# Kernel tuning notes

Measured on AMD Instinct MI355X. Metric: run time of the kernel, lower is better.

## Reference

```python
import jax, jax.numpy as jnp
import numpy as np

B, N, D, H = 4, 2048, 512, 8
HD = D // H


def setup_inputs() -> dict:
    key = jax.random.key(0)
    ks = jax.random.split(key, 12)
    s = 1.0 / np.sqrt(D)
    return {
        "node_feat": jax.random.normal(ks[0], (B, N, D), jnp.float32),
        "edge_weights": jax.random.uniform(ks[1], (B, N, N), jnp.float32),
        "adj_matrix": jax.random.uniform(ks[2], (B, N, N), jnp.float32),
        "masks": jnp.ones((B, N), jnp.float32),
        "class_token": 0.02 * jax.random.normal(ks[3], (1, 1, D), jnp.float32),
        "Wq": jax.random.uniform(ks[4], (D, D), jnp.float32, -s, s),
        "bq": jnp.zeros((D,), jnp.float32),
        "Wk": jax.random.uniform(ks[5], (D, D), jnp.float32, -s, s),
        "bk": jnp.zeros((D,), jnp.float32),
        "Wv": jax.random.uniform(ks[6], (D, D), jnp.float32, -s, s),
        "bv": jnp.zeros((D,), jnp.float32),
        "Wo": jax.random.uniform(ks[7], (D, D), jnp.float32, -s, s),
        "bo": jnp.zeros((D,), jnp.float32),
        "gamma": jnp.ones((D,), jnp.float32),
        "beta": jnp.zeros((D,), jnp.float32),
    }


def _attn_mask(edge_weights, masks):
    # inner block: edge gates + self-loops, clamped at 1
    inner = jnp.minimum(edge_weights + jnp.eye(N, dtype=edge_weights.dtype), 1.0)
    top = jnp.concatenate([jnp.ones((B, 1, 1), edge_weights.dtype), masks[:, None, :]], axis=2)  # [B,1,1+N]
    bot = jnp.concatenate([jnp.ones((B, N, 1), edge_weights.dtype), inner], axis=2)              # [B,N,1+N]
    m = jnp.concatenate([top, bot], axis=1)  # [B,1+N,1+N]
    ext = jnp.concatenate([jnp.ones((B, 1), masks.dtype), masks], axis=1)  # [B,1+N], CLS always valid
    return m * ext[:, None, :] * ext[:, :, None]


def reference(node_feat, edge_weights, adj_matrix, masks, class_token,
              Wq, bq, Wk, bk, Wv, bv, Wo, bo, gamma, beta):
    x = jnp.concatenate([jnp.broadcast_to(class_token, (B, 1, D)), node_feat], axis=1)  # [B,1+N,D]
    S = 1 + N
    q = (x @ Wq.T + bq).reshape(B, S, H, HD).transpose(0, 2, 1, 3)
    k = (x @ Wk.T + bk).reshape(B, S, H, HD).transpose(0, 2, 1, 3)
    v = (x @ Wv.T + bv).reshape(B, S, H, HD).transpose(0, 2, 1, 3)
    scores = jnp.einsum('bhqd,bhkd->bhqk', q, k) / jnp.sqrt(jnp.float32(HD))
    m = _attn_mask(edge_weights, masks)
    scores = jnp.where(m[:, None, :, :] == 0, jnp.float32(-1e9), scores)
    attn = jax.nn.softmax(scores, axis=-1)
    out = jnp.einsum('bhqk,bhkd->bhqd', attn, v).transpose(0, 2, 1, 3).reshape(B, S, D)
    out = out @ Wo.T + bo
    y = out + x
    mu = jnp.mean(y, axis=-1, keepdims=True)
    var = jnp.mean((y - mu) ** 2, axis=-1, keepdims=True)
    y = (y - mu) / jnp.sqrt(var + 1e-5) * gamma + beta
    return y[:, 0, :]
```

## Files before the change

### kernel.cpp

```cpp
#include <hip/hip_runtime.h>

#define B_ 4
#define N_ 2048
#define D_ 512
#define H_ 8
#define S_ (N_ + 1)
#define SC 32
#define NCH 65

#define Q0_OFF   0
#define TQ_OFF   1024
#define ATTN_OFF 8192
#define PW_OFF   81920
#define PZ_OFF   (PW_OFF + NCH * B_ * H_ * D_)
#define W_OFF    (PZ_OFF + NCH * B_ * H_ + 32)
#define O0_OFF   (W_OFF + B_ * H_ * D_)
#define Y_OFF    (O0_OFF + B_ * D_)

__device__ __forceinline__ float wave_reduce_sum(float v) {
    #pragma unroll
    for (int off = 32; off > 0; off >>= 1) v += __shfl_down(v, off, 64);
    return v;
}
__device__ __forceinline__ float wave_allreduce_sum(float v) {
    #pragma unroll
    for (int off = 1; off < 64; off <<= 1) v += __shfl_xor(v, off, 64);
    return v;
}

__global__ void q0_kernel(const float* __restrict__ ct,
                          const float* __restrict__ Wq, const float* __restrict__ bq,
                          float* __restrict__ ws) {
    int wv = threadIdx.x >> 6, lane = threadIdx.x & 63;
    int r = blockIdx.x * 8 + wv;
    const float4* c4 = (const float4*)ct;
    float4 ca = c4[lane * 2], cb = c4[lane * 2 + 1];
    const float4* row = (const float4*)(Wq + (size_t)r * D_);
    float4 a = row[lane * 2], b = row[lane * 2 + 1];
    float acc = a.x*ca.x + a.y*ca.y + a.z*ca.z + a.w*ca.w
              + b.x*cb.x + b.y*cb.y + b.z*cb.z + b.w*cb.w;
    acc = wave_reduce_sum(acc);
    if (lane == 0) ws[Q0_OFF + r] = acc + bq[r];
}

__global__ void tq_kernel(const float* __restrict__ Wk, float* __restrict__ ws) {
    int h = blockIdx.x, jc = blockIdx.y;
    int tid = threadIdx.x;
    __shared__ float q0s[64];
    if (tid < 64) q0s[tid] = ws[Q0_OFF + h * 64 + tid];
    __syncthreads();
    int j = jc * 128 + tid;
    float acc = 0.f;
    #pragma unroll 8
    for (int d2 = 0; d2 < 64; ++d2)
        acc += q0s[d2] * Wk[(size_t)(h * 64 + d2) * D_ + j];
    ws[TQ_OFF + h * D_ + j] = acc;
}

__global__ void __launch_bounds__(512)
scores_kernel(const float* __restrict__ nf, const float* __restrict__ ct,
              const float* __restrict__ masks, float* __restrict__ ws) {
    int b = blockIdx.y;
    int wv = threadIdx.x >> 6, lane = threadIdx.x & 63;
    int s = blockIdx.x * 8 + wv;
    if (s >= S_) return;
    const float* xrow = (s == 0) ? ct : (nf + ((size_t)b * N_ + (s - 1)) * D_);
    const float4* x4 = (const float4*)xrow;
    float4 xa = x4[lane];
    float4 xb = x4[64 + lane];
    float gate = 1.0f;
    if (s > 0) gate = (masks[b * N_ + s - 1] != 0.0f) ? 1.0f : 0.0f;
    const float4* t4 = (const float4*)(ws + TQ_OFF);
    float p[H_];
    #pragma unroll
    for (int h = 0; h < H_; ++h) {
        float4 ta = t4[h * 128 + lane], tb = t4[h * 128 + 64 + lane];
        p[h] = ta.x*xa.x + ta.y*xa.y + ta.z*xa.z + ta.w*xa.w
             + tb.x*xb.x + tb.y*xb.y + tb.z*xb.z + tb.w*xb.w;
        p[h] = wave_allreduce_sum(p[h]);
    }
    if (lane == 0) {
        #pragma unroll
        for (int h = 0; h < H_; ++h)
            ws[ATTN_OFF + (size_t)(b * H_ + h) * S_ + s] = gate * __expf(p[h] * 0.125f);
    }
}

__global__ void __launch_bounds__(512)
wsum_kernel(const float* __restrict__ nf, const float* __restrict__ ct,
            float* __restrict__ ws) {
    int chunk = blockIdx.x, b = blockIdx.y;
    int tid = threadIdx.x;
    __shared__ float sa[H_][SC];
    int s0 = chunk * SC;
    if (tid < H_ * SC) {
        int h = tid >> 5, ss = tid & 31;
        int s = s0 + ss;
        sa[h][ss] = (s < S_) ? ws[ATTN_OFF + (size_t)(b * H_ + h) * S_ + s] : 0.f;
    }
    __syncthreads();
    float acc[H_];
    #pragma unroll
    for (int h = 0; h < H_; ++h) acc[h] = 0.f;
    int smax = min(SC, S_ - s0);
    for (int ss = 0; ss < smax; ++ss) {
        int s = s0 + ss;
        const float* xrow = (s == 0) ? ct : (nf + ((size_t)b * N_ + (s - 1)) * D_);
        float xv = xrow[tid];
        #pragma unroll
        for (int h = 0; h < H_; ++h) acc[h] += sa[h][ss] * xv;
    }
    size_t base = ((size_t)chunk * B_ + b) * H_;
    #pragma unroll
    for (int h = 0; h < H_; ++h)
        ws[PW_OFF + (base + h) * D_ + tid] = acc[h];
    if (tid < H_) {
        float z = 0.f;
        #pragma unroll 8
        for (int ss = 0; ss < SC; ++ss) z += sa[tid][ss];
        ws[PZ_OFF + base + tid] = z;
    }
}

__global__ void reduce_w_kernel(float* __restrict__ ws) {
    int bh = blockIdx.x;
    int j = blockIdx.y * 128 + threadIdx.x;
    float z = 0.f;
    #pragma unroll 5
    for (int c = 0; c < NCH; ++c) z += ws[PZ_OFF + (size_t)(c * B_ * H_) + bh];
    float acc = 0.f;
    #pragma unroll 5
    for (int c = 0; c < NCH; ++c)
        acc += ws[PW_OFF + ((size_t)(c * B_ * H_) + bh) * D_ + j];
    ws[W_OFF + (size_t)bh * D_ + j] = acc / z;
}

__global__ void wv_kernel(const float* __restrict__ Wv, const float* __restrict__ bv,
                          float* __restrict__ ws) {
    int b = blockIdx.x;
    int wv = threadIdx.x >> 6, lane = threadIdx.x & 63;
    int r = blockIdx.y * 4 + wv;
    const float4* wrow = (const float4*)(ws + W_OFF + (size_t)b * H_ * D_ + (size_t)(r >> 6) * D_);
    float4 wa = wrow[lane * 2], wb = wrow[lane * 2 + 1];
    const float4* row = (const float4*)(Wv + (size_t)r * D_);
    float4 a = row[lane * 2], c = row[lane * 2 + 1];
    float acc = a.x*wa.x + a.y*wa.y + a.z*wa.z + a.w*wa.w
              + c.x*wb.x + c.y*wb.y + c.z*wb.z + c.w*wb.w;
    acc = wave_reduce_sum(acc);
    if (lane == 0) ws[O0_OFF + b * D_ + r] = acc + bv[r];
}

__global__ void wo_kernel(const float* __restrict__ Wo, const float* __restrict__ bo,
                          const float* __restrict__ ct, float* __restrict__ ws) {
    int b = blockIdx.x;
    int wv = threadIdx.x >> 6, lane = threadIdx.x & 63;
    int r = blockIdx.y * 4 + wv;
    const float4* ov = (const float4*)(ws + O0_OFF + (size_t)b * D_);
    float4 oa = ov[lane * 2], ob = ov[lane * 2 + 1];
    const float4* row = (const float4*)(Wo + (size_t)r * D_);
    float4 a = row[lane * 2], c = row[lane * 2 + 1];
    float acc = a.x*oa.x + a.y*oa.y + a.z*oa.z + a.w*oa.w
              + c.x*ob.x + c.y*ob.y + c.z*ob.z + c.w*ob.w;
    acc = wave_reduce_sum(acc);
    if (lane == 0) ws[Y_OFF + b * D_ + r] = acc + bo[r] + ct[r];
}

__global__ void ln_kernel(const float* __restrict__ gamma, const float* __restrict__ beta,
                          const float* __restrict__ ws, float* __restrict__ out) {
    int b = blockIdx.x;
    int tid = threadIdx.x, wv = tid >> 6, lane = tid & 63;
    float v = ws[Y_OFF + b * D_ + tid];
    float s1 = v, s2 = v * v;
    #pragma unroll
    for (int off = 32; off > 0; off >>= 1) {
        s1 += __shfl_down(s1, off, 64);
        s2 += __shfl_down(s2, off, 64);
    }
    __shared__ float r1[8], r2[8];
    if (lane == 0) { r1[wv] = s1; r2[wv] = s2; }
    __syncthreads();
    if (tid == 0) {
        float a = 0.f, c = 0.f;
        for (int i = 0; i < 8; ++i) { a += r1[i]; c += r2[i]; }
        r1[0] = a; r2[0] = c;
    }
    __syncthreads();
    float mean = r1[0] * (1.0f / D_);
    float var  = r2[0] * (1.0f / D_) - mean * mean;
    float rinv = rsqrtf(var + 1e-5f);
    out[b * D_ + tid] = (v - mean) * rinv * gamma[tid] + beta[tid];
}

extern "C" void kernel_launch(void* const* d_in, const int* in_sizes, int n_in,
                              void* d_out, int out_size, void* d_ws, size_t ws_size,
                              hipStream_t stream) {
    const float* nf    = (const float*)d_in[0];
    const float* masks = (const float*)d_in[3];
    const float* ct    = (const float*)d_in[4];
    const float* Wq    = (const float*)d_in[5];
    const float* bq    = (const float*)d_in[6];
    const float* Wk    = (const float*)d_in[7];
    const float* Wv    = (const float*)d_in[9];
    const float* bv    = (const float*)d_in[10];
    const float* Wo    = (const float*)d_in[11];
    const float* bo    = (const float*)d_in[12];
    const float* gamma = (const float*)d_in[13];
    const float* beta  = (const float*)d_in[14];
    float* ws  = (float*)d_ws;
    float* out = (float*)d_out;

    hipLaunchKernelGGL(q0_kernel, dim3(64), dim3(512), 0, stream, ct, Wq, bq, ws);
    hipLaunchKernelGGL(tq_kernel, dim3(H_, 4), dim3(128), 0, stream, Wk, ws);
    hipLaunchKernelGGL(scores_kernel, dim3(257, B_), dim3(512), 0, stream, nf, ct, masks, ws);
    hipLaunchKernelGGL(wsum_kernel, dim3(NCH, B_), dim3(512), 0, stream, nf, ct, ws);
    hipLaunchKernelGGL(reduce_w_kernel, dim3(B_ * H_, 4), dim3(128), 0, stream, ws);
    hipLaunchKernelGGL(wv_kernel, dim3(B_, 128), dim3(256), 0, stream, Wv, bv, ws);
    hipLaunchKernelGGL(wo_kernel, dim3(B_, 128), dim3(256), 0, stream, Wo, bo, ct, ws);
    hipLaunchKernelGGL(ln_kernel, dim3(B_), dim3(512), 0, stream, gamma, beta, ws, out);
}
```

Measured before the change: 189.0 us.

## Fuse all stages into one persistent kernel with software grid barriers

```diff
diff --git a/kernel.cpp b/kernel.cpp
--- a/kernel.cpp
+++ b/kernel.cpp
@@ -7,14 +7,15 @@
 #define S_ (N_ + 1)
 #define SC 32
 #define NCH 65
-
-#define Q0_OFF   0
+#define NB  260
+
+#define BAR_OFF  0
+#define Q0_OFF   64
 #define TQ_OFF   1024
 #define ATTN_OFF 8192
 #define PW_OFF   81920
 #define PZ_OFF   (PW_OFF + NCH * B_ * H_ * D_)
-#define W_OFF    (PZ_OFF + NCH * B_ * H_ + 32)
-#define O0_OFF   (W_OFF + B_ * H_ * D_)
+#define O0_OFF   (PZ_OFF + 2176)
 #define Y_OFF    (O0_OFF + B_ * D_)
 
 __device__ __forceinline__ float wave_reduce_sum(float v) {
@@ -27,168 +28,194 @@
     for (int off = 1; off < 64; off <<= 1) v += __shfl_xor(v, off, 64);
     return v;
 }
-
-__global__ void q0_kernel(const float* __restrict__ ct,
-                          const float* __restrict__ Wq, const float* __restrict__ bq,
-                          float* __restrict__ ws) {
-    int wv = threadIdx.x >> 6, lane = threadIdx.x & 63;
-    int r = blockIdx.x * 8 + wv;
-    const float4* c4 = (const float4*)ct;
-    float4 ca = c4[lane * 2], cb = c4[lane * 2 + 1];
-    const float4* row = (const float4*)(Wq + (size_t)r * D_);
-    float4 a = row[lane * 2], b = row[lane * 2 + 1];
-    float acc = a.x*ca.x + a.y*ca.y + a.z*ca.z + a.w*ca.w
-              + b.x*cb.x + b.y*cb.y + b.z*cb.z + b.w*cb.w;
-    acc = wave_reduce_sum(acc);
-    if (lane == 0) ws[Q0_OFF + r] = acc + bq[r];
-}
-
-__global__ void tq_kernel(const float* __restrict__ Wk, float* __restrict__ ws) {
-    int h = blockIdx.x, jc = blockIdx.y;
-    int tid = threadIdx.x;
-    __shared__ float q0s[64];
-    if (tid < 64) q0s[tid] = ws[Q0_OFF + h * 64 + tid];
-    __syncthreads();
-    int j = jc * 128 + tid;
-    float acc = 0.f;
-    #pragma unroll 8
-    for (int d2 = 0; d2 < 64; ++d2)
-        acc += q0s[d2] * Wk[(size_t)(h * 64 + d2) * D_ + j];
-    ws[TQ_OFF + h * D_ + j] = acc;
+__device__ __forceinline__ float dot8(float4 a, float4 b, float4 c, float4 d) {
+    return a.x*b.x + a.y*b.y + a.z*b.z + a.w*b.w
+         + c.x*d.x + c.y*d.y + c.z*d.z + c.w*d.w;
+}
+
+__device__ __forceinline__ void grid_barrier(unsigned* bar, unsigned tgt) {
+    __syncthreads();
+    if (threadIdx.x == 0) {
+        __threadfence();
+        __hip_atomic_fetch_add(bar, 1u, __ATOMIC_RELEASE, __HIP_MEMORY_SCOPE_AGENT);
+        while (__hip_atomic_load(bar, __ATOMIC_ACQUIRE, __HIP_MEMORY_SCOPE_AGENT) < tgt) {
+            __builtin_amdgcn_s_sleep(1);
+        }
+    }
+    __syncthreads();
+}
+
+__global__ void init_kernel(float* __restrict__ ws) {
+    if (threadIdx.x < 32) ((unsigned*)ws)[BAR_OFF + threadIdx.x] = 0u;
 }
 
 __global__ void __launch_bounds__(512)
-scores_kernel(const float* __restrict__ nf, const float* __restrict__ ct,
-              const float* __restrict__ masks, float* __restrict__ ws) {
-    int b = blockIdx.y;
-    int wv = threadIdx.x >> 6, lane = threadIdx.x & 63;
-    int s = blockIdx.x * 8 + wv;
-    if (s >= S_) return;
-    const float* xrow = (s == 0) ? ct : (nf + ((size_t)b * N_ + (s - 1)) * D_);
-    const float4* x4 = (const float4*)xrow;
-    float4 xa = x4[lane];
-    float4 xb = x4[64 + lane];
-    float gate = 1.0f;
-    if (s > 0) gate = (masks[b * N_ + s - 1] != 0.0f) ? 1.0f : 0.0f;
-    const float4* t4 = (const float4*)(ws + TQ_OFF);
-    float p[H_];
-    #pragma unroll
-    for (int h = 0; h < H_; ++h) {
-        float4 ta = t4[h * 128 + lane], tb = t4[h * 128 + 64 + lane];
-        p[h] = ta.x*xa.x + ta.y*xa.y + ta.z*xa.z + ta.w*xa.w
-             + tb.x*xb.x + tb.y*xb.y + tb.z*xb.z + tb.w*xb.w;
-        p[h] = wave_allreduce_sum(p[h]);
-    }
-    if (lane == 0) {
+fused_kernel(const float* __restrict__ nf, const float* __restrict__ ct,
+             const float* __restrict__ masks,
+             const float* __restrict__ Wq, const float* __restrict__ bq,
+             const float* __restrict__ Wk,
+             const float* __restrict__ Wv, const float* __restrict__ bv,
+             const float* __restrict__ Wo, const float* __restrict__ bo,
+             const float* __restrict__ gamma, const float* __restrict__ beta,
+             float* __restrict__ ws, float* __restrict__ out) {
+    __shared__ float smem[544];
+    const int blk  = blockIdx.x;
+    const int tid  = threadIdx.x;
+    const int wv   = tid >> 6, lane = tid & 63;
+    unsigned* bar  = (unsigned*)ws + BAR_OFF;
+    unsigned  tgt  = NB;
+
+    if (blk < 64) {
+        int r = blk * 8 + wv;
+        const float4* c4 = (const float4*)ct;
+        float4 ca = c4[lane * 2], cb = c4[lane * 2 + 1];
+        const float4* row = (const float4*)(Wq + (size_t)r * D_);
+        float4 a = row[lane * 2], b = row[lane * 2 + 1];
+        float acc = dot8(a, ca, b, cb);
+        acc = wave_reduce_sum(acc);
+        if (lane == 0) ws[Q0_OFF + r] = acc + bq[r];
+    }
+    grid_barrier(bar, tgt); tgt += NB;
+
+    if (blk < 32 && tid < 64) smem[tid] = ws[Q0_OFF + (blk >> 2) * 64 + tid];
+    __syncthreads();
+    if (blk < 32 && tid < 128) {
+        int h = blk >> 2, j = (blk & 3) * 128 + tid;
+        float acc = 0.f;
+        #pragma unroll 8
+        for (int d2 = 0; d2 < 64; ++d2)
+            acc += smem[d2] * Wk[(size_t)(h * 64 + d2) * D_ + j];
+        ws[TQ_OFF + h * D_ + j] = acc;
+    }
+    grid_barrier(bar, tgt); tgt += NB;
+
+    {
+        int gw = blk * 8 + wv;
+        const float4* t4 = (const float4*)(ws + TQ_OFF);
+        for (int b = 0; b < B_; ++b) {
+            if (gw < S_) {
+                int s = gw;
+                const float* xrow = (s == 0) ? ct : (nf + ((size_t)b * N_ + (s - 1)) * D_);
+                const float4* x4 = (const float4*)xrow;
+                float4 xa = x4[lane], xb = x4[64 + lane];
+                float gate = 1.0f;
+                if (s > 0) gate = (masks[b * N_ + s - 1] != 0.0f) ? 1.0f : 0.0f;
+                float p[H_];
+                #pragma unroll
+                for (int h = 0; h < H_; ++h) {
+                    float4 ta = t4[h * 128 + lane], tb = t4[h * 128 + 64 + lane];
+                    p[h] = dot8(ta, xa, tb, xb);
+                    p[h] = wave_allreduce_sum(p[h]);
+                }
+                if (lane == 0) {
+                    #pragma unroll
+                    for (int h = 0; h < H_; ++h)
+                        ws[ATTN_OFF + (size_t)(b * H_ + h) * S_ + s] = gate * __expf(p[h] * 0.125f);
+                }
+            }
+        }
+    }
+    grid_barrier(bar, tgt); tgt += NB;
+
+    {
+        int chunk = blk >> 2, b = blk & 3;
+        int s0 = chunk * SC;
+        if (tid < 256) {
+            int h = tid >> 5, ss = tid & 31;
+            int s = s0 + ss;
+            smem[tid] = (s < S_) ? ws[ATTN_OFF + (size_t)(b * H_ + h) * S_ + s] : 0.f;
+        }
+        __syncthreads();
+        float acc[H_];
+        #pragma unroll
+        for (int h = 0; h < H_; ++h) acc[h] = 0.f;
+        int smax = min(SC, S_ - s0);
+        for (int ss = 0; ss < smax; ++ss) {
+            int s = s0 + ss;
+            const float* xrow = (s == 0) ? ct : (nf + ((size_t)b * N_ + (s - 1)) * D_);
+            float xv = xrow[tid];
+            #pragma unroll
+            for (int h = 0; h < H_; ++h) acc[h] += smem[(h << 5) + ss] * xv;
+        }
+        size_t base = ((size_t)chunk * B_ + b) * H_;
         #pragma unroll
         for (int h = 0; h < H_; ++h)
-            ws[ATTN_OFF + (size_t)(b * H_ + h) * S_ + s] = gate * __expf(p[h] * 0.125f);
-    }
-}
-
-__global__ void __launch_bounds__(512)
-wsum_kernel(const float* __restrict__ nf, const float* __restrict__ ct,
-            float* __restrict__ ws) {
-    int chunk = blockIdx.x, b = blockIdx.y;
-    int tid = threadIdx.x;
-    __shared__ float sa[H_][SC];
-    int s0 = chunk * SC;
-    if (tid < H_ * SC) {
-        int h = tid >> 5, ss = tid & 31;
-        int s = s0 + ss;
-        sa[h][ss] = (s < S_) ? ws[ATTN_OFF + (size_t)(b * H_ + h) * S_ + s] : 0.f;
-    }
-    __syncthreads();
-    float acc[H_];
-    #pragma unroll
-    for (int h = 0; h < H_; ++h) acc[h] = 0.f;
-    int smax = min(SC, S_ - s0);
-    for (int ss = 0; ss < smax; ++ss) {
-        int s = s0 + ss;
-        const float* xrow = (s == 0) ? ct : (nf + ((size_t)b * N_ + (s - 1)) * D_);
-        float xv = xrow[tid];
+            ws[PW_OFF + (base + h) * D_ + tid] = acc[h];
+        if (tid < H_) {
+            float z = 0.f;
+            #pragma unroll 8
+            for (int ss = 0; ss < SC; ++ss) z += smem[(tid << 5) + ss];
+            ws[PZ_OFF + base + tid] = z;
+        }
+    }
+    grid_barrier(bar, tgt); tgt += NB;
+
+    if (blk < 256) {
+        int bh = blk >> 3;
+        int b = bh >> 3, h = bh & 7;
+        float acc = 0.f;
+        const float* pwp = ws + PW_OFF + (size_t)bh * D_ + tid;
+        #pragma unroll 5
+        for (int c = 0; c < NCH; ++c) acc += pwp[(size_t)c * (B_ * H_ * D_)];
+        smem[tid] = acc;
+        if (wv == 0) {
+            float z = ws[PZ_OFF + lane * (B_ * H_) + bh];
+            if (lane == 0) z += ws[PZ_OFF + 64 * (B_ * H_) + bh];
+            z = wave_allreduce_sum(z);
+            if (lane == 0) smem[512] = z;
+        }
+        (void)b; (void)h;
+    }
+    __syncthreads();
+    if (blk < 256) {
+        int bh = blk >> 3, b = bh >> 3, h = bh & 7, sub = blk & 7;
+        int r = h * 64 + sub * 8 + wv;
+        const float4* wrow = (const float4*)smem;
+        float4 wa = wrow[lane * 2], wb = wrow[lane * 2 + 1];
+        const float4* row = (const float4*)(Wv + (size_t)r * D_);
+        float4 a = row[lane * 2], c = row[lane * 2 + 1];
+        float acc = dot8(a, wa, c, wb);
+        acc = wave_reduce_sum(acc);
+        if (lane == 0) ws[O0_OFF + b * D_ + r] = acc / smem[512] + bv[r];
+    }
+    grid_barrier(bar, tgt); tgt += NB;
+
+    if (blk < 256) {
+        int b = blk >> 6;
+        int r = (blk & 63) * 8 + wv;
+        const float4* ov = (const float4*)(ws + O0_OFF + (size_t)b * D_);
+        float4 oa = ov[lane * 2], ob = ov[lane * 2 + 1];
+        const float4* row = (const float4*)(Wo + (size_t)r * D_);
+        float4 a = row[lane * 2], c = row[lane * 2 + 1];
+        float acc = dot8(a, oa, c, ob);
+        acc = wave_reduce_sum(acc);
+        if (lane == 0) ws[Y_OFF + b * D_ + r] = acc + bo[r] + ct[r];
+    }
+    grid_barrier(bar, tgt);
+
+    if (blk >= B_) return;
+    {
+        int b = blk;
+        float v = ws[Y_OFF + b * D_ + tid];
+        float s1 = v, s2 = v * v;
         #pragma unroll
-        for (int h = 0; h < H_; ++h) acc[h] += sa[h][ss] * xv;
-    }
-    size_t base = ((size_t)chunk * B_ + b) * H_;
-    #pragma unroll
-    for (int h = 0; h < H_; ++h)
-        ws[PW_OFF + (base + h) * D_ + tid] = acc[h];
-    if (tid < H_) {
-        float z = 0.f;
-        #pragma unroll 8
-        for (int ss = 0; ss < SC; ++ss) z += sa[tid][ss];
-        ws[PZ_OFF + base + tid] = z;
-    }
-}
-
-__global__ void reduce_w_kernel(float* __restrict__ ws) {
-    int bh = blockIdx.x;
-    int j = blockIdx.y * 128 + threadIdx.x;
-    float z = 0.f;
-    #pragma unroll 5
-    for (int c = 0; c < NCH; ++c) z += ws[PZ_OFF + (size_t)(c * B_ * H_) + bh];
-    float acc = 0.f;
-    #pragma unroll 5
-    for (int c = 0; c < NCH; ++c)
-        acc += ws[PW_OFF + ((size_t)(c * B_ * H_) + bh) * D_ + j];
-    ws[W_OFF + (size_t)bh * D_ + j] = acc / z;
-}
-
-__global__ void wv_kernel(const float* __restrict__ Wv, const float* __restrict__ bv,
-                          float* __restrict__ ws) {
-    int b = blockIdx.x;
-    int wv = threadIdx.x >> 6, lane = threadIdx.x & 63;
-    int r = blockIdx.y * 4 + wv;
-    const float4* wrow = (const float4*)(ws + W_OFF + (size_t)b * H_ * D_ + (size_t)(r >> 6) * D_);
-    float4 wa = wrow[lane * 2], wb = wrow[lane * 2 + 1];
-    const float4* row = (const float4*)(Wv + (size_t)r * D_);
-    float4 a = row[lane * 2], c = row[lane * 2 + 1];
-    float acc = a.x*wa.x + a.y*wa.y + a.z*wa.z + a.w*wa.w
-              + c.x*wb.x + c.y*wb.y + c.z*wb.z + c.w*wb.w;
-    acc = wave_reduce_sum(acc);
-    if (lane == 0) ws[O0_OFF + b * D_ + r] = acc + bv[r];
-}
-
-__global__ void wo_kernel(const float* __restrict__ Wo, const float* __restrict__ bo,
-                          const float* __restrict__ ct, float* __restrict__ ws) {
-    int b = blockIdx.x;
-    int wv = threadIdx.x >> 6, lane = threadIdx.x & 63;
-    int r = blockIdx.y * 4 + wv;
-    const float4* ov = (const float4*)(ws + O0_OFF + (size_t)b * D_);
-    float4 oa = ov[lane * 2], ob = ov[lane * 2 + 1];
-    const float4* row = (const float4*)(Wo + (size_t)r * D_);
-    float4 a = row[lane * 2], c = row[lane * 2 + 1];
-    float acc = a.x*oa.x + a.y*oa.y + a.z*oa.z + a.w*oa.w
-              + c.x*ob.x + c.y*ob.y + c.z*ob.z + c.w*ob.w;
-    acc = wave_reduce_sum(acc);
-    if (lane == 0) ws[Y_OFF + b * D_ + r] = acc + bo[r] + ct[r];
-}
-
-__global__ void ln_kernel(const float* __restrict__ gamma, const float* __restrict__ beta,
-                          const float* __restrict__ ws, float* __restrict__ out) {
-    int b = blockIdx.x;
-    int tid = threadIdx.x, wv = tid >> 6, lane = tid & 63;
-    float v = ws[Y_OFF + b * D_ + tid];
-    float s1 = v, s2 = v * v;
-    #pragma unroll
-    for (int off = 32; off > 0; off >>= 1) {
-        s1 += __shfl_down(s1, off, 64);
-        s2 += __shfl_down(s2, off, 64);
-    }
-    __shared__ float r1[8], r2[8];
-    if (lane == 0) { r1[wv] = s1; r2[wv] = s2; }
-    __syncthreads();
-    if (tid == 0) {
-        float a = 0.f, c = 0.f;
-        for (int i = 0; i < 8; ++i) { a += r1[i]; c += r2[i]; }
-        r1[0] = a; r2[0] = c;
-    }
-    __syncthreads();
-    float mean = r1[0] * (1.0f / D_);
-    float var  = r2[0] * (1.0f / D_) - mean * mean;
-    float rinv = rsqrtf(var + 1e-5f);
-    out[b * D_ + tid] = (v - mean) * rinv * gamma[tid] + beta[tid];
+        for (int off = 32; off > 0; off >>= 1) {
+            s1 += __shfl_down(s1, off, 64);
+            s2 += __shfl_down(s2, off, 64);
+        }
+        if (lane == 0) { smem[wv] = s1; smem[8 + wv] = s2; }
+        __syncthreads();
+        if (tid == 0) {
+            float a = 0.f, c = 0.f;
+            for (int i = 0; i < 8; ++i) { a += smem[i]; c += smem[8 + i]; }
+            smem[0] = a; smem[8] = c;
+        }
+        __syncthreads();
+        float mean = smem[0] * (1.0f / D_);
+        float var  = smem[8] * (1.0f / D_) - mean * mean;
+        float rinv = rsqrtf(var + 1e-5f);
+        out[b * D_ + tid] = (v - mean) * rinv * gamma[tid] + beta[tid];
+    }
 }
 
 extern "C" void kernel_launch(void* const* d_in, const int* in_sizes, int n_in,
@@ -209,12 +236,7 @@
     float* ws  = (float*)d_ws;
     float* out = (float*)d_out;
 
-    hipLaunchKernelGGL(q0_kernel, dim3(64), dim3(512), 0, stream, ct, Wq, bq, ws);
-    hipLaunchKernelGGL(tq_kernel, dim3(H_, 4), dim3(128), 0, stream, Wk, ws);
-    hipLaunchKernelGGL(scores_kernel, dim3(257, B_), dim3(512), 0, stream, nf, ct, masks, ws);
-    hipLaunchKernelGGL(wsum_kernel, dim3(NCH, B_), dim3(512), 0, stream, nf, ct, ws);
-    hipLaunchKernelGGL(reduce_w_kernel, dim3(B_ * H_, 4), dim3(128), 0, stream, ws);
-    hipLaunchKernelGGL(wv_kernel, dim3(B_, 128), dim3(256), 0, stream, Wv, bv, ws);
-    hipLaunchKernelGGL(wo_kernel, dim3(B_, 128), dim3(256), 0, stream, Wo, bo, ct, ws);
-    hipLaunchKernelGGL(ln_kernel, dim3(B_), dim3(512), 0, stream, gamma, beta, ws, out);
-}
+    hipLaunchKernelGGL(init_kernel, dim3(1), dim3(64), 0, stream, ws);
+    hipLaunchKernelGGL(fused_kernel, dim3(NB), dim3(512), 0, stream,
+                       nf, ct, masks, Wq, bq, Wk, Wv, bv, Wo, bo, gamma, beta, ws, out);
+}
```

After: 322.3 us. 70.5% more time.
